# Kernel optimization log

Hardware: AMD Instinct MI355X
Metric: run time of the kernel (lower is better)

Reference implementation:

```python
import jax, jax.numpy as jnp
import numpy as np

D = 1024
H = 16
K = D // H
B = 2
S = 2048

def setup_inputs() -> dict:
    key = jax.random.key(0)
    k1, k2, k3, k4, k5 = jax.random.split(key, 5)
    x = jax.random.normal(k1, (B, S, D), dtype=jnp.float32)
    # nn.Linear(d, 3d): weight [3d, d], bias [3d]
    Wqkv = jax.random.normal(k2, (3 * D, D), dtype=jnp.float32) / np.sqrt(D)
    bqkv = jax.random.normal(k3, (3 * D,), dtype=jnp.float32) * 0.01
    Wproj = jax.random.normal(k4, (D, D), dtype=jnp.float32) / np.sqrt(D)
    bproj = jax.random.normal(k5, (D,), dtype=jnp.float32) * 0.01
    return {"x": x, "Wqkv": Wqkv, "bqkv": bqkv, "Wproj": Wproj, "bproj": bproj}

def reference(x, Wqkv, bqkv, Wproj, bproj):
    Bsz, Slen, d = x.shape
    # fused QKV projection: [B,S,3d] -> [B,S,3,H,K] -> (3, B, H, S, K)
    qkv = (jnp.einsum('bsd,ed->bse', x, Wqkv) + bqkv).reshape(Bsz, Slen, 3, H, K)
    q, k, v = jnp.moveaxis(qkv, 2, 0).transpose(0, 1, 3, 2, 4)
    scale = 1.0 / jnp.sqrt(jnp.asarray(K, dtype=x.dtype))
    scores = jnp.einsum('bhqk,bhmk->bhqm', q, k) * scale  # [B,H,S,S]
    a = jax.nn.softmax(scores, axis=-1)
    # dropout is identity in eval mode
    o = jnp.einsum('bhqm,bhmk->bhqk', a, v)  # [B,H,S,K]
    o = o.transpose(0, 2, 1, 3).reshape(Bsz, Slen, d)
    return jnp.einsum('bsd,ed->bse', o, Wproj) + bproj
```

## Files before the change

### kernel.cpp

```cpp
#include <hip/hip_runtime.h>
#include <cstdint>

typedef unsigned short ushort_t;
typedef short short8 __attribute__((ext_vector_type(8)));
typedef float f32x4 __attribute__((ext_vector_type(4)));
typedef float float4v __attribute__((ext_vector_type(4)));
typedef unsigned int uint2v __attribute__((ext_vector_type(2)));

#define DDIM 1024
#define HH 16
#define HEADK 64
#define BB 2
#define SS 2048

#if __has_builtin(__builtin_amdgcn_exp2f)
#define EXP2F(x) __builtin_amdgcn_exp2f(x)
#else
#define EXP2F(x) exp2f(x)
#endif

__device__ __forceinline__ ushort_t f2bf(float f) {
  union { float f; uint32_t u; } c; c.f = f;
  uint32_t u = c.u;
  u += 0x7fffu + ((u >> 16) & 1u);
  return (ushort_t)(u >> 16);
}

__device__ __forceinline__ uint32_t pkbf_trunc(float a, float b) {
  union { float f; uint32_t u; } ca, cb;
  ca.f = a; cb.f = b;
  return __builtin_amdgcn_perm(cb.u, ca.u, 0x07060302);
}

__device__ __forceinline__ uint32_t pkbf_rne(float a, float b) {
  return (uint32_t)f2bf(a) | ((uint32_t)f2bf(b) << 16);
}

__device__ __forceinline__ float bfhi2f(uint32_t u) {
  union { uint32_t u; float f; } c; c.u = u & 0xffff0000u; return c.f;
}
__device__ __forceinline__ float bflo2f(uint32_t u) {
  union { uint32_t u; float f; } c; c.u = u << 16; return c.f;
}

__device__ __forceinline__ void glds16(const ushort_t* gp, ushort_t* lp) {
  __builtin_amdgcn_global_load_lds(
      (const __attribute__((address_space(1))) uint32_t*)gp,
      (__attribute__((address_space(3))) uint32_t*)lp, 16, 0, 0);
}

__global__ void cvt3_kernel(const float* __restrict__ s0, ushort_t* __restrict__ d0, int n0,
                            const float* __restrict__ s1, ushort_t* __restrict__ d1, int n1,
                            const float* __restrict__ s2, ushort_t* __restrict__ d2, int n2) {
  int i = blockIdx.x * blockDim.x + threadIdx.x;
  const float* src; ushort_t* dst; int k;
  if (i < n0) { src = s0; dst = d0; k = i; }
  else if (i < n0 + n1) { src = s1; dst = d1; k = i - n0; }
  else if (i < n0 + n1 + n2) { src = s2; dst = d2; k = i - n0 - n1; }
  else return;
  float4v v = ((const float4v*)src)[k];
  uint2v o; o[0] = pkbf_rne(v[0], v[1]); o[1] = pkbf_rne(v[2], v[3]);
  ((uint2v*)dst)[k] = o;
}

template <int MODE, int TM>
__global__ __launch_bounds__(256) void gemm_nt(
    const ushort_t* __restrict__ A, const ushort_t* __restrict__ Bm,
    const float* __restrict__ bias, float* __restrict__ Cout,
    ushort_t* __restrict__ Cbf, int M, int N, int Kd) {
  __shared__ ushort_t smem[128 * 64 * 2];
  ushort_t* As = smem;
  ushort_t* Bs = smem + TM * 64;
  const int MI = TM / 32;
  const int tid = threadIdx.x;
  const int wv = tid >> 6, lane = tid & 63;
  const int l15 = lane & 15, quad = lane >> 4;
  const int wm = wv >> 1, wn = wv & 1;
  const int tm0 = blockIdx.y * TM, tn0 = blockIdx.x * 128;

  f32x4 acc[MI][4];
#pragma unroll
  for (int i = 0; i < MI; ++i)
#pragma unroll
    for (int j = 0; j < 4; ++j) acc[i][j] = (f32x4){0.f, 0.f, 0.f, 0.f};

  const int lrow = lane >> 3;
  const int gcb = (lane & 7) ^ lrow;
  const int ACI = TM / 32;

  for (int k0 = 0; k0 < Kd; k0 += 64) {
#pragma unroll
    for (int c = 0; c < ACI; ++c) {
      int seg = wv * ACI + c;
      glds16(A + (size_t)(tm0 + seg * 8 + lrow) * Kd + k0 + gcb * 8,
             As + seg * 512);
    }
#pragma unroll
    for (int c = 0; c < 4; ++c) {
      int seg = wv * 4 + c;
      glds16(Bm + (size_t)(tn0 + seg * 8 + lrow) * Kd + k0 + gcb * 8,
             Bs + seg * 512);
    }
    __syncthreads();
#pragma unroll
    for (int kk = 0; kk < 64; kk += 32) {
      short8 af[MI], bfr[4];
#pragma unroll
      for (int i = 0; i < MI; ++i) {
        int r = wm * (TM / 2) + i * 16 + l15;
        int cb = (kk >> 3) + quad;
        af[i] = *(const short8*)(As + r * 64 + ((cb ^ (l15 & 7)) << 3));
      }
#pragma unroll
      for (int j = 0; j < 4; ++j) {
        int r = wn * 64 + j * 16 + l15;
        int cb = (kk >> 3) + quad;
        bfr[j] = *(const short8*)(Bs + r * 64 + ((cb ^ (l15 & 7)) << 3));
      }
#pragma unroll
      for (int i = 0; i < MI; ++i)
#pragma unroll
        for (int j = 0; j < 4; ++j)
          acc[i][j] = __builtin_amdgcn_mfma_f32_16x16x32_bf16(
              af[i], bfr[j], acc[i][j], 0, 0, 0);
    }
    __syncthreads();
  }

  if (MODE == 1) {
#pragma unroll
    for (int j = 0; j < 4; ++j) {
      int col = tn0 + wn * 64 + j * 16 + l15;
      float bv = bias[col];
#pragma unroll
      for (int i = 0; i < MI; ++i) {
        int row0 = tm0 + wm * (TM / 2) + i * 16 + quad * 4;
#pragma unroll
        for (int r = 0; r < 4; ++r)
          Cout[(size_t)(row0 + r) * N + col] = acc[i][j][r] + bv;
      }
    }
  } else {
    const int t = tn0 >> 10;
    if (t < 2) {
#pragma unroll
      for (int j = 0; j < 4; ++j) {
        int col = tn0 + wn * 64 + j * 16 + l15;
        float bv = bias[col];
        int hh = (col >> 6) & 15, kk2 = col & 63;
#pragma unroll
        for (int i = 0; i < MI; ++i) {
          int row0 = tm0 + wm * (TM / 2) + i * 16 + quad * 4;
#pragma unroll
          for (int r = 0; r < 4; ++r) {
            int row = row0 + r;
            int b = row >> 11, s = row & 2047;
            float v = acc[i][j][r] + bv;
            if (t == 0) v *= 0.18033688f;
            size_t base =
                (((size_t)t * BB + b) * HH + hh) * ((size_t)SS * HEADK);
            Cbf[base + (size_t)s * HEADK + kk2] = f2bf(v);
          }
        }
      }
    } else {
      __syncthreads();
#pragma unroll
      for (int j = 0; j < 4; ++j) {
        int c = wn * 64 + j * 16 + l15;
        float bv = bias[tn0 + c];
#pragma unroll
        for (int i = 0; i < MI; ++i) {
          int row0 = wm * (TM / 2) + i * 16 + quad * 4;
          uint2v dw;
          dw[0] = pkbf_rne(acc[i][j][0] + bv, acc[i][j][1] + bv);
          dw[1] = pkbf_rne(acc[i][j][2] + bv, acc[i][j][3] + bv);
          int rb = row0 >> 3;
          *(uint2v*)(&smem[c * 128 + (((rb ^ (c & 15)) << 3) | (row0 & 7))]) =
              dw;
        }
      }
      __syncthreads();
      const int rb2 = lane & 15;
      const int cg = lane >> 4;
#pragma unroll
      for (int it = 0; it < 8; ++it) {
        int c = wv * 32 + it * 4 + cg;
        short8 vv = *(const short8*)(&smem[c * 128 + ((rb2 ^ (c & 15)) << 3)]);
        int gcol = tn0 + c;
        int hh = (gcol >> 6) & 15, kk2 = gcol & 63;
        int grow = tm0 + rb2 * 8;
        int b = grow >> 11, s = grow & 2047;
        size_t base = (((size_t)2 * BB + b) * HH + hh) * ((size_t)SS * HEADK);
        *(short8*)(&Cbf[base + (size_t)kk2 * SS + s]) = vv;
      }
    }
  }
}

template <int NSPLIT>
__global__ __launch_bounds__(256, 4) void attn_kernel(
    const ushort_t* __restrict__ qkv, ushort_t* __restrict__ O0,
    ushort_t* __restrict__ O1, float* __restrict__ Lp) {
  constexpr int NT = (SS / NSPLIT) / 32;
  __shared__ ushort_t Kt[3][32 * 64];
  __shared__ ushort_t Vt[3][64 * 32];
  __shared__ ushort_t Pw[4][2][32 * 32];

  const int qt = blockIdx.x, h = blockIdx.y;
  const int b = blockIdx.z / NSPLIT, ns = blockIdx.z % NSPLIT;
  const int tid = threadIdx.x;
  const int wv = tid >> 6, lane = tid & 63;
  const int l15 = lane & 15, quad = lane >> 4;

  const size_t hstride = (size_t)SS * HEADK;
  const ushort_t* Qg = qkv + ((size_t)(0 * BB + b) * HH + h) * hstride;
  const ushort_t* Kg = qkv + ((size_t)(1 * BB + b) * HH + h) * hstride;
  const ushort_t* Vg = qkv + ((size_t)(2 * BB + b) * HH + h) * hstride;
  ushort_t* Opp = ns ? O1 : O0;

  short8 qf[2][2];
#pragma unroll
  for (int mi = 0; mi < 2; ++mi)
#pragma unroll
    for (int kc = 0; kc < 2; ++kc)
      qf[mi][kc] = *(const short8*)(
          Qg + (size_t)(qt * 128 + wv * 32 + mi * 16 + l15) * 64 + kc * 32 +
          quad * 8);

  const short ONE = (short)0x3F80;
  short8 ones = {ONE, ONE, ONE, ONE, ONE, ONE, ONE, ONE};

  f32x4 oat[2][4];
  f32x4 loa[2];
#pragma unroll
  for (int mi = 0; mi < 2; ++mi) {
    loa[mi] = (f32x4){0.f, 0.f, 0.f, 0.f};
#pragma unroll
    for (int c = 0; c < 4; ++c) oat[mi][c] = (f32x4){0.f, 0.f, 0.f, 0.f};
  }

  const int lrow = lane >> 3, gcb = (lane & 7) ^ lrow;
  const int vfl = lane >> 2;
  const int vgb = (lane & 3) ^ ((vfl >> 1) & 3);

  const int pos0 = ns * (SS / NSPLIT);

  auto stage = [&](int jj, int db) {
    glds16(Kg + (size_t)(pos0 + jj * 32 + wv * 8 + lrow) * 64 + gcb * 8,
           &Kt[db][wv * 512]);
    glds16(Vg + (size_t)(wv * 16 + vfl) * SS + pos0 + jj * 32 + vgb * 8,
           &Vt[db][wv * 512]);
  };

  auto qk_phase = [&](int kb, int pb) {
    f32x4 st[2][2];
    __builtin_amdgcn_s_setprio(1);
#pragma unroll
    for (int cf = 0; cf < 2; ++cf) {
      int n = cf * 16 + l15;
      short8 kf0 = *(const short8*)(&Kt[kb][n * 64 + ((quad ^ (n & 7)) << 3)]);
      short8 kf1 =
          *(const short8*)(&Kt[kb][n * 64 + (((quad + 4) ^ (n & 7)) << 3)]);
#pragma unroll
      for (int mi = 0; mi < 2; ++mi) {
        f32x4 z = (f32x4){0.f, 0.f, 0.f, 0.f};
        z = __builtin_amdgcn_mfma_f32_16x16x32_bf16(kf0, qf[mi][0], z, 0, 0, 0);
        z = __builtin_amdgcn_mfma_f32_16x16x32_bf16(kf1, qf[mi][1], z, 0, 0, 0);
        st[mi][cf] = z;
      }
    }
    __builtin_amdgcn_s_setprio(0);
#pragma unroll
    for (int mi = 0; mi < 2; ++mi)
#pragma unroll
      for (int cf = 0; cf < 2; ++cf) {
        float e0 = EXP2F(st[mi][cf][0]);
        float e1 = EXP2F(st[mi][cf][1]);
        float e2 = EXP2F(st[mi][cf][2]);
        float e3 = EXP2F(st[mi][cf][3]);
        uint2v dw;
        dw[0] = pkbf_trunc(e0, e1);
        dw[1] = pkbf_trunc(e2, e3);
        int row = mi * 16 + l15;
        int pbv = 2 * cf + (quad >> 1);
        int pbs = pbv ^ ((l15 >> 1) & 3);
        *(uint2v*)(&Pw[wv][pb][row * 32 + pbs * 8 + (quad & 1) * 4]) = dw;
      }
  };

  stage(0, 0);
  stage(1, 1);

  asm volatile("s_waitcnt vmcnt(2)" ::: "memory");
  __builtin_amdgcn_s_barrier();
  asm volatile("" ::: "memory");
  __builtin_amdgcn_sched_barrier(0);
  qk_phase(0, 0);

  int vb = 0;
  for (int j = 0; j < NT; ++j) {
    const int kb = (vb == 2) ? 0 : vb + 1;
    const int sb = (kb == 2) ? 0 : kb + 1;
    asm volatile("s_waitcnt vmcnt(0)" ::: "memory");
    __builtin_amdgcn_s_barrier();
    asm volatile("" ::: "memory");
    __builtin_amdgcn_sched_barrier(0);

    if (j + 2 < NT) stage(j + 2, sb);
    if (j + 1 < NT) qk_phase(kb, (j + 1) & 1);

    short8 pa[2];
#pragma unroll
    for (int mi = 0; mi < 2; ++mi) {
      int row = mi * 16 + l15;
      pa[mi] = *(const short8*)(&Pw[wv][j & 1][row * 32 +
                                              ((quad ^ ((l15 >> 1) & 3)) << 3)]);
    }
    __builtin_amdgcn_s_setprio(1);
#pragma unroll
    for (int cf = 0; cf < 4; ++cf) {
      short8 vf = *(const short8*)(&Vt[vb][(cf * 16 + l15) * 32 +
                                           ((quad ^ ((l15 >> 1) & 3)) << 3)]);
#pragma unroll
      for (int mi = 0; mi < 2; ++mi)
        oat[mi][cf] = __builtin_amdgcn_mfma_f32_16x16x32_bf16(
            vf, pa[mi], oat[mi][cf], 0, 0, 0);
    }
#pragma unroll
    for (int mi = 0; mi < 2; ++mi)
      loa[mi] = __builtin_amdgcn_mfma_f32_16x16x32_bf16(ones, pa[mi], loa[mi],
                                                        0, 0, 0);
    __builtin_amdgcn_s_setprio(0);

    vb = kb;
  }

  const size_t obase = ((size_t)b * HH + h) * SS * HEADK;
#pragma unroll
  for (int mi = 0; mi < 2; ++mi) {
#pragma unroll
    for (int cf = 0; cf < 4; ++cf) {
      uint2v dw;
      dw[0] = pkbf_rne(oat[mi][cf][0], oat[mi][cf][1]);
      dw[1] = pkbf_rne(oat[mi][cf][2], oat[mi][cf][3]);
      int cb = 2 * cf + (quad >> 1);
      int cbs = cb ^ (l15 & 7);
      *(uint2v*)(&Pw[wv][0][l15 * 64 + cbs * 8 + (quad & 1) * 4]) = dw;
    }
    const int r = lane >> 2;
#pragma unroll
    for (int pass = 0; pass < 2; ++pass) {
      int g = (lane & 3) + 4 * pass;
      short8 ov = *(const short8*)(&Pw[wv][0][r * 64 + ((g ^ (r & 7)) << 3)]);
      int qrow = qt * 128 + wv * 32 + mi * 16 + r;
      *(short8*)(&Opp[obase + (size_t)qrow * 64 + g * 8]) = ov;
    }
    if (quad == 0) {
      int qrow = qt * 128 + wv * 32 + mi * 16 + l15;
      Lp[((size_t)(ns * BB + b) * HH + h) * SS + qrow] = loa[mi][0];
    }
  }
}

template <int NSPLIT>
__global__ void reduce_kernel(const ushort_t* __restrict__ O0,
                              const ushort_t* __restrict__ O1,
                              const float* __restrict__ Lp,
                              ushort_t* __restrict__ ob) {
  const size_t nsL = (size_t)BB * HH * SS;
  int c = blockIdx.x * blockDim.x + threadIdx.x;
  int fc = c & 7;
  int hh = (c >> 3) & 15;
  int row = c >> 7;
  int b = row >> 11, s = row & 2047;
  size_t po = (((size_t)b * HH + hh) * SS + s) * 64 + fc * 8;
  size_t lo = ((size_t)b * HH + hh) * SS + s;
  const ushort_t* Ops[2] = {O0, O1};
  float acc[8];
#pragma unroll
  for (int i = 0; i < 8; ++i) acc[i] = 0.f;
  float l = 0.f;
#pragma unroll
  for (int t = 0; t < NSPLIT; ++t) {
    uint2v a0 = *(const uint2v*)(&Ops[t][po]);
    uint2v a1 = *(const uint2v*)(&Ops[t][po + 4]);
    acc[0] += bflo2f(a0[0]); acc[1] += bfhi2f(a0[0]);
    acc[2] += bflo2f(a0[1]); acc[3] += bfhi2f(a0[1]);
    acc[4] += bflo2f(a1[0]); acc[5] += bfhi2f(a1[0]);
    acc[6] += bflo2f(a1[1]); acc[7] += bfhi2f(a1[1]);
    l += Lp[(size_t)t * nsL + lo];
  }
  float inv = 1.0f / l;
  uint2v o0, o1;
  o0[0] = pkbf_rne(acc[0] * inv, acc[1] * inv);
  o0[1] = pkbf_rne(acc[2] * inv, acc[3] * inv);
  o1[0] = pkbf_rne(acc[4] * inv, acc[5] * inv);
  o1[1] = pkbf_rne(acc[6] * inv, acc[7] * inv);
  size_t oo = ((size_t)(b * SS + s)) * DDIM + hh * 64 + fc * 8;
  *(uint2v*)(&ob[oo]) = o0;
  *(uint2v*)(&ob[oo + 4]) = o1;
}

extern "C" void kernel_launch(void* const* d_in, const int* in_sizes, int n_in,
                              void* d_out, int out_size, void* d_ws,
                              size_t ws_size, hipStream_t stream) {
  const float* x = (const float*)d_in[0];
  const float* Wqkv = (const float*)d_in[1];
  const float* bqkv = (const float*)d_in[2];
  const float* Wproj = (const float*)d_in[3];
  const float* bproj = (const float*)d_in[4];
  float* out = (float*)d_out;

  ushort_t* xb = (ushort_t*)d_ws;
  ushort_t* wqb = xb + (size_t)4096 * 1024;
  ushort_t* wpb = wqb + (size_t)3072 * 1024;
  ushort_t* qkvb = wpb + (size_t)1024 * 1024;
  ushort_t* Op1 = qkvb + (size_t)3 * BB * HH * SS * HEADK;
  ushort_t* Op0 = xb;
  float* Lp = (float*)wqb;
  ushort_t* obuf = qkvb;

  const int n0 = 4096 * 1024 / 4, n1 = 3072 * 1024 / 4, n2 = 1024 * 1024 / 4;
  cvt3_kernel<<<(n0 + n1 + n2 + 255) / 256, 256, 0, stream>>>(
      x, xb, n0, Wqkv, wqb, n1, Wproj, wpb, n2);
  gemm_nt<0, 128><<<dim3(3072 / 128, 4096 / 128), 256, 0, stream>>>(
      xb, wqb, bqkv, nullptr, qkvb, 4096, 3072, 1024);
  attn_kernel<2><<<dim3(16, 16, BB * 2), 256, 0, stream>>>(qkvb, Op0, Op1, Lp);
  reduce_kernel<2><<<(BB * SS * DDIM / 8) / 256, 256, 0, stream>>>(Op0, Op1,
                                                                   Lp, obuf);
  gemm_nt<1, 64><<<dim3(1024 / 128, 4096 / 64), 256, 0, stream>>>(
      obuf, wpb, bproj, out, nullptr, 4096, 1024, 1024);
}
```

Before: 193.4 us.

## Replace QKV GEMM with 256x256-tile, 512-thread double-buffered kernel

Adds a dedicated QKV projection GEMM that uses 256x256 output tiles with 8 waves and double-buffered LDS loads through global_load_lds, with explicit vmcnt waits, barriers and s_setprio around the MFMA blocks. The aim is more data reuse per LDS byte and overlap of global loads with MFMA work, compared with the previous 128x128 tile with no double buffering. The epilogue keeps the same Q/K/V scatter and transposed-V store, but uses per-wave LDS slabs. The trade-off is only 192 workgroups (fewer than on a 256-CU part), 128 KB of LDS per block, and heavy register pressure from 32 accumulators per thread.

```diff
diff --git a/kernel.cpp b/kernel.cpp
--- a/kernel.cpp
+++ b/kernel.cpp
@@ -61,6 +61,142 @@
   float4v v = ((const float4v*)src)[k];
   uint2v o; o[0] = pkbf_rne(v[0], v[1]); o[1] = pkbf_rne(v[2], v[3]);
   ((uint2v*)dst)[k] = o;
+}
+
+__global__ __launch_bounds__(512, 2) void gemm_qkv(
+    const ushort_t* __restrict__ A, const ushort_t* __restrict__ Bm,
+    const float* __restrict__ bias, ushort_t* __restrict__ Cbf) {
+  constexpr int Kd = 1024;
+  __shared__ ushort_t smem[65536];
+  const int tid = threadIdx.x;
+  const int wv = tid >> 6, lane = tid & 63;
+  const int l15 = lane & 15, quad = lane >> 4;
+  const int wm = wv >> 2, wn = wv & 3;
+  const int tm0 = blockIdx.y * 256, tn0 = blockIdx.x * 256;
+  const int lrow = lane >> 3;
+  const int gcb = (lane & 7) ^ lrow;
+
+  f32x4 acc[8][4];
+#pragma unroll
+  for (int i = 0; i < 8; ++i)
+#pragma unroll
+    for (int j = 0; j < 4; ++j) acc[i][j] = (f32x4){0.f, 0.f, 0.f, 0.f};
+
+  auto stage = [&](int t, int buf) {
+    ushort_t* As = smem + buf * 32768;
+    ushort_t* Bs = As + 16384;
+    const int k0 = t * 64;
+#pragma unroll
+    for (int c = 0; c < 4; ++c) {
+      int seg = wv * 4 + c;
+      glds16(A + (size_t)(tm0 + seg * 8 + lrow) * Kd + k0 + gcb * 8,
+             As + seg * 512);
+      glds16(Bm + (size_t)(tn0 + seg * 8 + lrow) * Kd + k0 + gcb * 8,
+             Bs + seg * 512);
+    }
+  };
+
+  stage(0, 0);
+  for (int t = 0; t < 16; ++t) {
+    const int cur = t & 1;
+    asm volatile("" ::: "memory");
+    __builtin_amdgcn_s_barrier();
+    if (t + 1 < 16) {
+      stage(t + 1, cur ^ 1);
+      asm volatile("s_waitcnt vmcnt(8)" ::: "memory");
+    } else {
+      asm volatile("s_waitcnt vmcnt(0)" ::: "memory");
+    }
+    __builtin_amdgcn_s_barrier();
+    asm volatile("" ::: "memory");
+    __builtin_amdgcn_sched_barrier(0);
+
+    const ushort_t* As = smem + cur * 32768;
+    const ushort_t* Bs = As + 16384;
+    short8 bfr[4][2];
+#pragma unroll
+    for (int j = 0; j < 4; ++j)
+#pragma unroll
+      for (int kc = 0; kc < 2; ++kc) {
+        int n = wn * 64 + j * 16 + l15;
+        bfr[j][kc] =
+            *(const short8*)(Bs + n * 64 + (((kc * 4 + quad) ^ (l15 & 7)) << 3));
+      }
+#pragma unroll
+    for (int q = 0; q < 4; ++q) {
+      short8 af[2][2];
+#pragma unroll
+      for (int i2 = 0; i2 < 2; ++i2)
+#pragma unroll
+        for (int kc = 0; kc < 2; ++kc) {
+          int r = wm * 128 + (q * 2 + i2) * 16 + l15;
+          af[i2][kc] =
+              *(const short8*)(As + r * 64 + (((kc * 4 + quad) ^ (l15 & 7)) << 3));
+        }
+      __builtin_amdgcn_s_setprio(1);
+#pragma unroll
+      for (int kc = 0; kc < 2; ++kc)
+#pragma unroll
+        for (int i2 = 0; i2 < 2; ++i2)
+#pragma unroll
+          for (int j = 0; j < 4; ++j)
+            acc[q * 2 + i2][j] = __builtin_amdgcn_mfma_f32_16x16x32_bf16(
+                af[i2][kc], bfr[j][kc], acc[q * 2 + i2][j], 0, 0, 0);
+      __builtin_amdgcn_s_setprio(0);
+    }
+  }
+
+  const int tsel = tn0 >> 10;
+  if (tsel < 2) {
+#pragma unroll
+    for (int j = 0; j < 4; ++j) {
+      int col = tn0 + wn * 64 + j * 16 + l15;
+      float bv = bias[col];
+      int hh = (col >> 6) & 15, kk2 = col & 63;
+#pragma unroll
+      for (int mi = 0; mi < 8; ++mi) {
+        int row0 = tm0 + wm * 128 + mi * 16 + quad * 4;
+#pragma unroll
+        for (int r = 0; r < 4; ++r) {
+          int row = row0 + r;
+          int b = row >> 11, s = row & 2047;
+          float v = acc[mi][j][r] + bv;
+          if (tsel == 0) v *= 0.18033688f;
+          size_t base = (((size_t)tsel * BB + b) * HH + hh) * ((size_t)SS * HEADK);
+          Cbf[base + (size_t)s * HEADK + kk2] = f2bf(v);
+        }
+      }
+    }
+  } else {
+    __builtin_amdgcn_s_barrier();
+    ushort_t* slab = smem + wv * 8192;
+#pragma unroll
+    for (int j = 0; j < 4; ++j) {
+      int c = j * 16 + l15;
+      float bv = bias[tn0 + wn * 64 + c];
+#pragma unroll
+      for (int mi = 0; mi < 8; ++mi) {
+        int row0 = mi * 16 + quad * 4;
+        uint2v dw;
+        dw[0] = pkbf_rne(acc[mi][j][0] + bv, acc[mi][j][1] + bv);
+        dw[1] = pkbf_rne(acc[mi][j][2] + bv, acc[mi][j][3] + bv);
+        int rb = row0 >> 3;
+        *(uint2v*)(&slab[c * 128 + (((rb ^ (c & 15)) << 3) | (row0 & 7))]) = dw;
+      }
+    }
+    const int r2 = lane & 15, cg = lane >> 4;
+#pragma unroll
+    for (int it = 0; it < 16; ++it) {
+      int c = it * 4 + cg;
+      short8 vv = *(const short8*)(&slab[c * 128 + ((r2 ^ (c & 15)) << 3)]);
+      int gcol = tn0 + wn * 64 + c;
+      int hh = (gcol >> 6) & 15, kk2 = gcol & 63;
+      int grow = tm0 + wm * 128 + r2 * 8;
+      int b = grow >> 11, s = grow & 2047;
+      size_t base = (((size_t)2 * BB + b) * HH + hh) * ((size_t)SS * HEADK);
+      *(short8*)(&Cbf[base + (size_t)kk2 * SS + s]) = vv;
+    }
+  }
 }
 
 template <int MODE, int TM>
@@ -138,61 +274,6 @@
 #pragma unroll
         for (int r = 0; r < 4; ++r)
           Cout[(size_t)(row0 + r) * N + col] = acc[i][j][r] + bv;
-      }
-    }
-  } else {
-    const int t = tn0 >> 10;
-    if (t < 2) {
-#pragma unroll
-      for (int j = 0; j < 4; ++j) {
-        int col = tn0 + wn * 64 + j * 16 + l15;
-        float bv = bias[col];
-        int hh = (col >> 6) & 15, kk2 = col & 63;
-#pragma unroll
-        for (int i = 0; i < MI; ++i) {
-          int row0 = tm0 + wm * (TM / 2) + i * 16 + quad * 4;
-#pragma unroll
-          for (int r = 0; r < 4; ++r) {
-            int row = row0 + r;
-            int b = row >> 11, s = row & 2047;
-            float v = acc[i][j][r] + bv;
-            if (t == 0) v *= 0.18033688f;
-            size_t base =
-                (((size_t)t * BB + b) * HH + hh) * ((size_t)SS * HEADK);
-            Cbf[base + (size_t)s * HEADK + kk2] = f2bf(v);
-          }
-        }
-      }
-    } else {
-      __syncthreads();
-#pragma unroll
-      for (int j = 0; j < 4; ++j) {
-        int c = wn * 64 + j * 16 + l15;
-        float bv = bias[tn0 + c];
-#pragma unroll
-        for (int i = 0; i < MI; ++i) {
-          int row0 = wm * (TM / 2) + i * 16 + quad * 4;
-          uint2v dw;
-          dw[0] = pkbf_rne(acc[i][j][0] + bv, acc[i][j][1] + bv);
-          dw[1] = pkbf_rne(acc[i][j][2] + bv, acc[i][j][3] + bv);
-          int rb = row0 >> 3;
-          *(uint2v*)(&smem[c * 128 + (((rb ^ (c & 15)) << 3) | (row0 & 7))]) =
-              dw;
-        }
-      }
-      __syncthreads();
-      const int rb2 = lane & 15;
-      const int cg = lane >> 4;
-#pragma unroll
-      for (int it = 0; it < 8; ++it) {
-        int c = wv * 32 + it * 4 + cg;
-        short8 vv = *(const short8*)(&smem[c * 128 + ((rb2 ^ (c & 15)) << 3)]);
-        int gcol = tn0 + c;
-        int hh = (gcol >> 6) & 15, kk2 = gcol & 63;
-        int grow = tm0 + rb2 * 8;
-        int b = grow >> 11, s = grow & 2047;
-        size_t base = (((size_t)2 * BB + b) * HH + hh) * ((size_t)SS * HEADK);
-        *(short8*)(&Cbf[base + (size_t)kk2 * SS + s]) = vv;
       }
     }
   }
@@ -424,8 +505,8 @@
   const int n0 = 4096 * 1024 / 4, n1 = 3072 * 1024 / 4, n2 = 1024 * 1024 / 4;
   cvt3_kernel<<<(n0 + n1 + n2 + 255) / 256, 256, 0, stream>>>(
       x, xb, n0, Wqkv, wqb, n1, Wproj, wpb, n2);
-  gemm_nt<0, 128><<<dim3(3072 / 128, 4096 / 128), 256, 0, stream>>>(
-      xb, wqb, bqkv, nullptr, qkvb, 4096, 3072, 1024);
+  gemm_qkv<<<dim3(3072 / 256, 4096 / 256), 512, 0, stream>>>(xb, wqb, bqkv,
+                                                             qkvb);
   attn_kernel<2><<<dim3(16, 16, BB * 2), 256, 0, stream>>>(qkvb, Op0, Op1, Lp);
   reduce_kernel<2><<<(BB * SS * DDIM / 8) / 256, 256, 0, stream>>>(Op0, Op1,
                                                                    Lp, obuf);
```

After: 186.0 us. -3.8%, faster.
